# Kernel optimization log

Hardware: AMD Instinct MI355X
Metric: run time of the kernel (lower is better)

## Reference

```python
import jax, jax.numpy as jnp
import numpy as np

NT, NTR, NQ = 2048, 4096, 257  # time samples, traces, quantile knots


def cumtrapz(y, dx):
    # cumulative trapezoid along last axis, zero-prepended (preserve_dims=True)
    c = jnp.cumsum((y[..., 1:] + y[..., :-1]) * (0.5 * dx), axis=-1)
    return jnp.concatenate([jnp.zeros_like(y[..., :1]), c], axis=-1)


def trapz(y, dx):
    return (jnp.sum(y, axis=-1) - 0.5 * (y[..., 0] + y[..., -1])) * dx


def renorm(f, dx):
    # square + normalize to a pdf along time (standard W2-FWI renormalization)
    g = f * f
    return g / trapz(g, dx)[..., None]


def true_quantile(pdf, x, p, dx):
    # step-function quantile: invert clipped CDF via searchsorted per trace
    cdf = jnp.clip(cumtrapz(pdf, dx), 0.0, 1.0)  # [B, nt]
    idx = jax.vmap(lambda c: jnp.searchsorted(c, p))(cdf)  # [B, nq]
    idx = jnp.clip(idx, 0, x.shape[0] - 1)
    return x[idx]  # [B, nq]


def natural_cubic_coeffs(p, q):
    # batched natural cubic spline of q(p); knots p shared across batch
    h = p[1:] - p[:-1]                                 # [n-1]
    slope = (q[..., 1:] - q[..., :-1]) / h             # [B, n-1]
    rhs = 6.0 * (slope[..., 1:] - slope[..., :-1])     # [B, n-2]
    diag = 2.0 * (h[:-1] + h[1:])
    off = h[1:-1]
    T = jnp.diag(diag) + jnp.diag(off, 1) + jnp.diag(off, -1)  # [n-2, n-2], shared
    M_inner = jnp.linalg.solve(T, rhs[..., None])[..., 0]      # [B, n-2]
    z = jnp.zeros_like(q[..., :1])
    M = jnp.concatenate([z, M_inner, z], axis=-1)      # natural BCs: M0 = Mn = 0
    a = q[..., :-1]
    b = slope - h * (2.0 * M[..., :-1] + M[..., 1:]) / 6.0
    c = 0.5 * M[..., :-1]
    d = (M[..., 1:] - M[..., :-1]) / (6.0 * h)
    return a, b, c, d  # each [B, n-1]


def spline_eval(p, a, b, c, d, tq):
    # vectorized batched spline evaluation (replaces per-element Python loop)
    idx = jnp.clip(jnp.searchsorted(p, tq, side='left') - 1, 0, p.shape[0] - 2)
    frac = tq - p[idx]
    ga = jnp.take_along_axis(a, idx, axis=-1)
    gb = jnp.take_along_axis(b, idx, axis=-1)
    gc = jnp.take_along_axis(c, idx, axis=-1)
    gd = jnp.take_along_axis(d, idx, axis=-1)
    return ga + frac * (gb + frac * (gc + frac * gd))


def w2_forward(f, obs_data, t, p):
    dx = t[1] - t[0]
    # constructor-time part: quantile splines of observed data
    q = true_quantile(renorm(obs_data, dx), t, p, dx)   # [B, nq]
    a, b, c, d = natural_cubic_coeffs(p, q)
    # forward: CDF of synthetic, composed with observed quantile
    F = cumtrapz(renorm(f, dx), dx)                     # [B, nt]
    off_diag = spline_eval(p, a, b, c, d, F)            # [B, nt]
    diff = (t[None, :] - off_diag) ** 2
    integrated = trapz(diff * f, dx)                    # [B]
    return jnp.sum(integrated)


def setup_inputs() -> dict:
    key = jax.random.key(0)
    k1, k2 = jax.random.split(key)
    f = jax.random.normal(k1, (NTR, NT), dtype=jnp.float32)
    obs_data = jax.random.normal(k2, (NTR, NT), dtype=jnp.float32)
    t = jnp.linspace(0.0, 2.0, NT, dtype=jnp.float32)
    p = jnp.linspace(0.0, 1.0, NQ, dtype=jnp.float32)
    return {"f": f, "obs_data": obs_data, "t": t, "p": p}


def reference(f, obs_data, t, p):
    return w2_forward(f, obs_data, t, p)
```

## Files before the change

### kernel.cpp

```cpp
#include <hip/hip_runtime.h>

#define TPB 256
#define NT_ 2048
#define NQ_ 257
#define EPT 8
#define BW 16
#define BD (2*BW+1)
#define BAND_BYTES (BD*256*4)
#define H_P 0.00390625f
#define RTPB 1024

__device__ __forceinline__ double shfl_down_f64(double x, int off) {
  union { double d; int i[2]; } u; u.d = x;
  u.i[0] = __shfl_down(u.i[0], off, 64);
  u.i[1] = __shfl_down(u.i[1], off, 64);
  return u.d;
}

template<int CTRL, int RM, int BM, bool BC>
__device__ __forceinline__ float dppf(float x) {
  return __int_as_float(__builtin_amdgcn_update_dpp(
      0, __float_as_int(x), CTRL, RM, BM, BC));
}
template<int CTRL, int RM, int BM, bool BC>
__device__ __forceinline__ double dppd(double x) {
  union { double d; int i[2]; } u, o; u.d = x;
  o.i[0] = __builtin_amdgcn_update_dpp(0, u.i[0], CTRL, RM, BM, BC);
  o.i[1] = __builtin_amdgcn_update_dpp(0, u.i[1], CTRL, RM, BM, BC);
  return o.d;
}
__device__ __forceinline__ void iscan2(float& a, float& b) {
  a += dppf<0x111,0xF,0xF,true >(a);  b += dppf<0x111,0xF,0xF,true >(b);
  a += dppf<0x112,0xF,0xF,true >(a);  b += dppf<0x112,0xF,0xF,true >(b);
  a += dppf<0x114,0xF,0xF,true >(a);  b += dppf<0x114,0xF,0xF,true >(b);
  a += dppf<0x118,0xF,0xF,true >(a);  b += dppf<0x118,0xF,0xF,true >(b);
  a += dppf<0x142,0xa,0xF,false>(a);  b += dppf<0x142,0xa,0xF,false>(b);
  a += dppf<0x143,0xc,0xF,false>(a);  b += dppf<0x143,0xc,0xF,false>(b);
}
__device__ __forceinline__ void iscan2d(double& a, double& b) {
  a += dppd<0x111,0xF,0xF,true >(a);  b += dppd<0x111,0xF,0xF,true >(b);
  a += dppd<0x112,0xF,0xF,true >(a);  b += dppd<0x112,0xF,0xF,true >(b);
  a += dppd<0x114,0xF,0xF,true >(a);  b += dppd<0x114,0xF,0xF,true >(b);
  a += dppd<0x118,0xF,0xF,true >(a);  b += dppd<0x118,0xF,0xF,true >(b);
  a += dppd<0x142,0xa,0xF,false>(a);  b += dppd<0x142,0xa,0xF,false>(b);
  a += dppd<0x143,0xc,0xF,false>(a);  b += dppd<0x143,0xc,0xF,false>(b);
}

__global__ void w2_setup(float* __restrict__ bandS) {
  __shared__ double sh_L[256];
  __shared__ double sh_winv[256];
  const int tid = threadIdx.x;
  if (tid < 255) {
    double d, dm;
    if (tid >= 20) {
      d = dm = 3.7320508075688772935;
    } else {
      d = 4.0; dm = 0.0;
      for (int i = 1; i <= tid; i++) { dm = d; d = 4.0 - 1.0 / d; }
    }
    sh_winv[tid] = 256.0 / d;
    sh_L[tid] = (tid == 0) ? 0.0 : 1.0 / dm;
  }
  __syncthreads();
  const int j = tid;
  const double H = (double)H_P;
  if (j < 255) {
    double y[BW + 1];
    y[0] = 1.0;
    #pragma unroll
    for (int m = 1; m <= BW; m++) {
      int i = j + m;
      y[m] = (i <= 254) ? (-sh_L[i] * y[m - 1]) : 0.0;
    }
    double xn = 0.0;
    #pragma unroll
    for (int m = BW; m >= 0; m--) {
      int i = j + m;
      double val = 0.0;
      if (i <= 254) {
        double num = y[m] - ((i < 254) ? H * xn : 0.0);
        val = num * sh_winv[i];
        xn = val;
      }
      bandS[(m + BW) * 256 + j] = (float)val;
    }
    #pragma unroll
    for (int m = -1; m >= -BW; m--) {
      int i = j + m;
      double val = 0.0;
      if (i >= 0) {
        val = (-H * xn) * sh_winv[i];
        xn = val;
      }
      bandS[(m + BW) * 256 + j] = (float)val;
    }
  } else {
    for (int mm = 0; mm < BD; mm++) bandS[mm * 256 + j] = 0.0f;
  }
}

__global__ __launch_bounds__(TPB) void w2_main(
    const float* __restrict__ f, const float* __restrict__ obs,
    const float* __restrict__ t, const float* __restrict__ bandS,
    double* __restrict__ row_out) {
  __shared__ float s_qA[NQ_], s_qB[NQ_];
  __shared__ float s_rhsA[255 + 2 * BW], s_rhsB[255 + 2 * BW];
  __shared__ float s_MA[NQ_], s_MB[NQ_];
  __shared__ float4 s_coefA[256], s_coefB[256];
  __shared__ float s_wfA[4], s_wfB[4], s_wf2A[4], s_wf2B[4];
  __shared__ double s_wdA[4], s_wdB[4];
  __shared__ double s_miscA[2], s_miscB[2];

  const int tid = threadIdx.x;
  const int lane = tid & 63;
  const int wid = tid >> 6;
  const int rowA = (int)blockIdx.x * 2;
  const int rowB = rowA + 1;
  const int base = tid * EPT;
  const int emax = (tid == TPB - 1) ? EPT - 1 : EPT;

  const double dx = (double)t[1] - (double)t[0];

  float tl[EPT + 1];
  {
    const float4 a = *reinterpret_cast<const float4*>(t + base);
    const float4 b = *reinterpret_cast<const float4*>(t + base + 4);
    tl[0] = a.x; tl[1] = a.y; tl[2] = a.z; tl[3] = a.w;
    tl[4] = b.x; tl[5] = b.y; tl[6] = b.z; tl[7] = b.w;
  }
  tl[EPT] = (tid < TPB - 1) ? t[base + EPT] : 0.0f;

  float sAA[EPT], sAB[EPT];
  float epA = 0.0f, epB = 0.0f;
  {
    const float* orA = obs + (size_t)rowA * NT_;
    const float* orB = obs + (size_t)rowB * NT_;
    float ovA[EPT + 1], ovB[EPT + 1];
    {
      const float4 a0 = *reinterpret_cast<const float4*>(orA + base);
      const float4 a1 = *reinterpret_cast<const float4*>(orA + base + 4);
      const float4 b0 = *reinterpret_cast<const float4*>(orB + base);
      const float4 b1 = *reinterpret_cast<const float4*>(orB + base + 4);
      ovA[0] = a0.x; ovA[1] = a0.y; ovA[2] = a0.z; ovA[3] = a0.w;
      ovA[4] = a1.x; ovA[5] = a1.y; ovA[6] = a1.z; ovA[7] = a1.w;
      ovB[0] = b0.x; ovB[1] = b0.y; ovB[2] = b0.z; ovB[3] = b0.w;
      ovB[4] = b1.x; ovB[5] = b1.y; ovB[6] = b1.z; ovB[7] = b1.w;
    }
    ovA[EPT] = (tid < TPB - 1) ? orA[base + EPT] : 0.0f;
    ovB[EPT] = (tid < TPB - 1) ? orB[base + EPT] : 0.0f;
    for (int k = 0; k < emax; k++) {
      sAA[k] = ovA[k] * ovA[k] + ovA[k + 1] * ovA[k + 1];
      sAB[k] = ovB[k] * ovB[k] + ovB[k + 1] * ovB[k + 1];
      epA += sAA[k];
      epB += sAB[k];
    }
    if (emax < EPT) { sAA[EPT - 1] = 0.0f; sAB[EPT - 1] = 0.0f; }
  }
  float vA = epA, vB = epB;
  iscan2(vA, vB);
  float exclA = __shfl_up(vA, 1, 64);
  float exclB = __shfl_up(vB, 1, 64);
  if (lane == 0) { exclA = 0.0f; exclB = 0.0f; }
  if (lane == 63) { s_wfA[wid] = vA; s_wfB[wid] = vB; }
  __syncthreads();
  float woffA = 0.0f, totA = 0.0f, woffB = 0.0f, totB = 0.0f;
  #pragma unroll
  for (int w = 0; w < 4; w++) {
    float swA = s_wfA[w], swB = s_wfB[w];
    if (w < wid) { woffA += swA; woffB += swB; }
    totA += swA; totB += swB;
  }
  float runA = woffA + exclA, inclA = woffA + vA, invA = 1.0f / totA;
  float runB = woffB + exclB, inclB = woffB + vB, invB = 1.0f / totB;

  {
    float cprev = fminf(runA * invA, 1.0f);
    int j = (int)(cprev * 256.0f) + 1;
    float r = runA;
    for (int k = 0; k < emax; k++) {
      float cu_uns = (k == emax - 1) ? inclA : (r + sAA[k]);
      r = cu_uns;
      float cuc = fminf(cu_uns * invA, 1.0f);
      int jh = (int)(cuc * 256.0f);
      float tq = tl[k + 1];
      for (; j <= jh; j++) s_qA[j] = tq;
    }
    if (tid == 0) s_qA[0] = tl[0];
    if (tid == TPB - 1) {
      float tq = tl[EPT - 1];
      for (; j <= 256; j++) s_qA[j] = tq;
    }
  }
  {
    float cprev = fminf(runB * invB, 1.0f);
    int j = (int)(cprev * 256.0f) + 1;
    float r = runB;
    for (int k = 0; k < emax; k++) {
      float cu_uns = (k == emax - 1) ? inclB : (r + sAB[k]);
      r = cu_uns;
      float cuc = fminf(cu_uns * invB, 1.0f);
      int jh = (int)(cuc * 256.0f);
      float tq = tl[k + 1];
      for (; j <= jh; j++) s_qB[j] = tq;
    }
    if (tid == 0) s_qB[0] = tl[0];
    if (tid == TPB - 1) {
      float tq = tl[EPT - 1];
      for (; j <= 256; j++) s_qB[j] = tq;
    }
  }

  const float* frA = f + (size_t)rowA * NT_;
  const float* frB = f + (size_t)rowB * NT_;
  float fvA[EPT + 1], fvB[EPT + 1];
  {
    const float4 a0 = *reinterpret_cast<const float4*>(frA + base);
    const float4 a1 = *reinterpret_cast<const float4*>(frA + base + 4);
    const float4 b0 = *reinterpret_cast<const float4*>(frB + base);
    const float4 b1 = *reinterpret_cast<const float4*>(frB + base + 4);
    fvA[0] = a0.x; fvA[1] = a0.y; fvA[2] = a0.z; fvA[3] = a0.w;
    fvA[4] = a1.x; fvA[5] = a1.y; fvA[6] = a1.z; fvA[7] = a1.w;
    fvB[0] = b0.x; fvB[1] = b0.y; fvB[2] = b0.z; fvB[3] = b0.w;
    fvB[4] = b1.x; fvB[5] = b1.y; fvB[6] = b1.z; fvB[7] = b1.w;
  }
  fvA[EPT] = (tid < TPB - 1) ? frA[base + EPT] : 0.0f;
  fvB[EPT] = (tid < TPB - 1) ? frB[base + EPT] : 0.0f;

  float sBA[EPT], sBB[EPT];
  float ep2A = 0.0f, ep2B = 0.0f;
  for (int k = 0; k < emax; k++) {
    sBA[k] = fvA[k] * fvA[k] + fvA[k + 1] * fvA[k + 1];
    sBB[k] = fvB[k] * fvB[k] + fvB[k + 1] * fvB[k + 1];
    ep2A += sBA[k];
    ep2B += sBB[k];
  }
  if (emax < EPT) { sBA[EPT - 1] = 0.0f; sBB[EPT - 1] = 0.0f; }
  float v2A = ep2A, v2B = ep2B;
  iscan2(v2A, v2B);
  float excl2A = __shfl_up(v2A, 1, 64);
  float excl2B = __shfl_up(v2B, 1, 64);
  if (lane == 0) { excl2A = 0.0f; excl2B = 0.0f; }
  if (lane == 63) { s_wf2A[wid] = v2A; s_wf2B[wid] = v2B; }
  __syncthreads();

  float woff2A = 0.0f, tot2A = 0.0f, woff2B = 0.0f, tot2B = 0.0f;
  #pragma unroll
  for (int w = 0; w < 4; w++) {
    float swA = s_wf2A[w], swB = s_wf2B[w];
    if (w < wid) { woff2A += swA; woff2B += swB; }
    tot2A += swA; tot2B += swB;
  }
  float run2A = woff2A + excl2A, inv2A = 1.0f / tot2A;
  float run2B = woff2B + excl2B, inv2B = 1.0f / tot2B;

  if (tid < 255) {
    float sl0A = (s_qA[tid + 1] - s_qA[tid]) * 256.0f;
    float sl1A = (s_qA[tid + 2] - s_qA[tid + 1]) * 256.0f;
    s_rhsA[BW + tid] = 6.0f * (sl1A - sl0A);
    float sl0B = (s_qB[tid + 1] - s_qB[tid]) * 256.0f;
    float sl1B = (s_qB[tid + 2] - s_qB[tid + 1]) * 256.0f;
    s_rhsB[BW + tid] = 6.0f * (sl1B - sl0B);
  }
  if (tid < BW) { s_rhsA[tid] = 0.0f; s_rhsB[tid] = 0.0f; }
  if (tid >= TPB - BW) {
    s_rhsA[tid + (2 * BW - 1)] = 0.0f;
    s_rhsB[tid + (2 * BW - 1)] = 0.0f;
  }
  __syncthreads();

  float MregA = 0.0f, MregB = 0.0f;
  if (tid < 255) {
    #pragma unroll 11
    for (int dd = 0; dd < BD; dd++) {
      float w = bandS[dd * 256 + tid];
      MregA += w * s_rhsA[tid + dd];
      MregB += w * s_rhsB[tid + dd];
    }
  }
  if (tid < 255) { s_MA[tid + 1] = MregA; s_MB[tid + 1] = MregB; }
  if (tid == 0) { s_MA[0] = 0.0f; s_MA[256] = 0.0f; s_MB[0] = 0.0f; s_MB[256] = 0.0f; }
  __syncthreads();

  {
    const float h = H_P;
    float q0A = s_qA[tid], q1A = s_qA[tid + 1];
    float MiA = s_MA[tid], Mi1A = s_MA[tid + 1];
    float slA = (q1A - q0A) * 256.0f;
    float bA = slA - h * (2.0f * MiA + Mi1A) * (1.0f / 6.0f);
    s_coefA[tid] = make_float4(q0A, bA, 0.5f * MiA, (Mi1A - MiA) * (256.0f / 6.0f));
    float q0B = s_qB[tid], q1B = s_qB[tid + 1];
    float MiB = s_MB[tid], Mi1B = s_MB[tid + 1];
    float slB = (q1B - q0B) * 256.0f;
    float bB = slB - h * (2.0f * MiB + Mi1B) * (1.0f / 6.0f);
    s_coefB[tid] = make_float4(q0B, bB, 0.5f * MiB, (Mi1B - MiB) * (256.0f / 6.0f));
  }
  __syncthreads();

  double wsumA = 0.0, wsumB = 0.0;
  {
    float r2A = run2A, r2B = run2B;
    #pragma unroll
    for (int k = 0; k < EPT; k++) {
      if (k > 0) { r2A += sBA[k - 1]; r2B += sBB[k - 1]; }
      float FA = r2A * inv2A;
      float FB = r2B * inv2B;
      int idxA = (int)ceilf(FA * 256.0f) - 1;
      int idxB = (int)ceilf(FB * 256.0f) - 1;
      if (idxA < 0) idxA = 0; if (idxA > 255) idxA = 255;
      if (idxB < 0) idxB = 0; if (idxB > 255) idxB = 255;
      float fracA = FA - (float)idxA * H_P;
      float fracB = FB - (float)idxB * H_P;
      float4 cfA = s_coefA[idxA];
      float4 cfB = s_coefB[idxB];
      float valA = cfA.x + fracA * (cfA.y + fracA * (cfA.z + fracA * cfA.w));
      float valB = cfB.x + fracB * (cfB.y + fracB * (cfB.z + fracB * cfB.w));
      float diffA = tl[k] - valA;
      float diffB = tl[k] - valB;
      float wvA = diffA * diffA * fvA[k];
      float wvB = diffB * diffB * fvB[k];
      if (tid == 0 && k == 0) { s_miscA[0] = (double)wvA; s_miscB[0] = (double)wvB; }
      if (tid == TPB - 1 && k == EPT - 1) { s_miscA[1] = (double)wvA; s_miscB[1] = (double)wvB; }
      wsumA += (double)wvA;
      wsumB += (double)wvB;
    }
  }
  double rA = wsumA, rB = wsumB;
  iscan2d(rA, rB);
  if (lane == 63) { s_wdA[wid] = rA; s_wdB[wid] = rB; }
  __syncthreads();
  if (tid == 0) {
    double totwA = s_wdA[0] + s_wdA[1] + s_wdA[2] + s_wdA[3];
    double totwB = s_wdB[0] + s_wdB[1] + s_wdB[2] + s_wdB[3];
    row_out[rowA] = (totwA - 0.5 * (s_miscA[0] + s_miscA[1])) * dx;
    row_out[rowB] = (totwB - 0.5 * (s_miscB[0] + s_miscB[1])) * dx;
  }
}

__global__ __launch_bounds__(RTPB) void w2_reduce(const double* __restrict__ row_out,
                                                  int ntr, float* __restrict__ out) {
  __shared__ double s[RTPB / 64];
  int tid = threadIdx.x, lane = tid & 63, wid = tid >> 6;
  double v = 0.0;
  for (int i = tid; i < ntr; i += RTPB) v += row_out[i];
  #pragma unroll
  for (int off = 32; off >= 1; off >>= 1) v += shfl_down_f64(v, off);
  if (lane == 0) s[wid] = v;
  __syncthreads();
  if (tid == 0) {
    double tot = 0.0;
    #pragma unroll
    for (int i = 0; i < RTPB / 64; i++) tot += s[i];
    out[0] = (float)tot;
  }
}

extern "C" void kernel_launch(void* const* d_in, const int* in_sizes, int n_in,
                              void* d_out, int out_size, void* d_ws, size_t ws_size,
                              hipStream_t stream) {
  const float* f   = (const float*)d_in[0];
  const float* obs = (const float*)d_in[1];
  const float* t   = (const float*)d_in[2];
  int nt = in_sizes[2];
  int ntr = in_sizes[0] / nt;

  float* bandS = (float*)d_ws;
  double* rows = (double*)((char*)d_ws + BAND_BYTES);

  hipLaunchKernelGGL(w2_setup, dim3(1), dim3(256), 0, stream, bandS);
  hipLaunchKernelGGL(w2_main, dim3(ntr / 2), dim3(TPB), 0, stream,
                     f, obs, t, bandS, rows);
  hipLaunchKernelGGL(w2_reduce, dim3(1), dim3(RTPB), 0, stream,
                     rows, ntr, (float*)d_out);
}
```

Baseline: 42.38 us.

## Precompute banded inverse at compile time, halve bandwidth, accumulate weights in float

The banded approximate inverse of the spline tridiagonal matrix is now built at compile time with constexpr and stored in constant memory, so the separate setup kernel launch is gone. The band half-width drops from 16 to 8, which halves the per-thread multiply-adds in the spline second-derivative solve, and that loop is now fully unrolled. Per-thread weighted sums are accumulated in float instead of double, saving conversions and FP64 adds. The risks are extra truncation error from the narrower band (off-diagonal decay factor about 0.27 per step) and slightly lower accumulation precision.

Result: faster. 36.29 us (-14.4%).

```diff
diff --git a/kernel.cpp b/kernel.cpp
--- a/kernel.cpp
+++ b/kernel.cpp
@@ -4,11 +4,55 @@
 #define NT_ 2048
 #define NQ_ 257
 #define EPT 8
-#define BW 16
+#define BW 8
 #define BD (2*BW+1)
-#define BAND_BYTES (BD*256*4)
 #define H_P 0.00390625f
 #define RTPB 1024
+
+struct Band { float v[BD * 256]; };
+constexpr Band make_band() {
+  Band b{};
+  double L[256] = {}, winv[256] = {};
+  const double H = 1.0 / 256.0;
+  double w = 4.0 * H;
+  winv[0] = 1.0 / w;
+  L[0] = 0.0;
+  for (int i = 1; i < 255; i++) {
+    L[i] = H * winv[i - 1];
+    w = 4.0 * H - L[i] * H;
+    winv[i] = 1.0 / w;
+  }
+  for (int j = 0; j < 255; j++) {
+    double y[BW + 1] = {};
+    y[0] = 1.0;
+    for (int m = 1; m <= BW; m++) {
+      int i = j + m;
+      y[m] = (i <= 254) ? (-L[i] * y[m - 1]) : 0.0;
+    }
+    double xn = 0.0;
+    for (int m = BW; m >= 0; m--) {
+      int i = j + m;
+      double val = 0.0;
+      if (i <= 254) {
+        double num = y[m] - ((i < 254) ? H * xn : 0.0);
+        val = num * winv[i];
+        xn = val;
+      }
+      b.v[(m + BW) * 256 + j] = (float)val;
+    }
+    for (int m = -1; m >= -BW; m--) {
+      int i = j + m;
+      double val = 0.0;
+      if (i >= 0) {
+        val = (-H * xn) * winv[i];
+        xn = val;
+      }
+      b.v[(m + BW) * 256 + j] = (float)val;
+    }
+  }
+  return b;
+}
+__device__ __constant__ Band g_band = make_band();
 
 __device__ __forceinline__ double shfl_down_f64(double x, int off) {
   union { double d; int i[2]; } u; u.d = x;
@@ -46,63 +90,9 @@
   a += dppd<0x143,0xc,0xF,false>(a);  b += dppd<0x143,0xc,0xF,false>(b);
 }
 
-__global__ void w2_setup(float* __restrict__ bandS) {
-  __shared__ double sh_L[256];
-  __shared__ double sh_winv[256];
-  const int tid = threadIdx.x;
-  if (tid < 255) {
-    double d, dm;
-    if (tid >= 20) {
-      d = dm = 3.7320508075688772935;
-    } else {
-      d = 4.0; dm = 0.0;
-      for (int i = 1; i <= tid; i++) { dm = d; d = 4.0 - 1.0 / d; }
-    }
-    sh_winv[tid] = 256.0 / d;
-    sh_L[tid] = (tid == 0) ? 0.0 : 1.0 / dm;
-  }
-  __syncthreads();
-  const int j = tid;
-  const double H = (double)H_P;
-  if (j < 255) {
-    double y[BW + 1];
-    y[0] = 1.0;
-    #pragma unroll
-    for (int m = 1; m <= BW; m++) {
-      int i = j + m;
-      y[m] = (i <= 254) ? (-sh_L[i] * y[m - 1]) : 0.0;
-    }
-    double xn = 0.0;
-    #pragma unroll
-    for (int m = BW; m >= 0; m--) {
-      int i = j + m;
-      double val = 0.0;
-      if (i <= 254) {
-        double num = y[m] - ((i < 254) ? H * xn : 0.0);
-        val = num * sh_winv[i];
-        xn = val;
-      }
-      bandS[(m + BW) * 256 + j] = (float)val;
-    }
-    #pragma unroll
-    for (int m = -1; m >= -BW; m--) {
-      int i = j + m;
-      double val = 0.0;
-      if (i >= 0) {
-        val = (-H * xn) * sh_winv[i];
-        xn = val;
-      }
-      bandS[(m + BW) * 256 + j] = (float)val;
-    }
-  } else {
-    for (int mm = 0; mm < BD; mm++) bandS[mm * 256 + j] = 0.0f;
-  }
-}
-
 __global__ __launch_bounds__(TPB) void w2_main(
     const float* __restrict__ f, const float* __restrict__ obs,
-    const float* __restrict__ t, const float* __restrict__ bandS,
-    double* __restrict__ row_out) {
+    const float* __restrict__ t, double* __restrict__ row_out) {
   __shared__ float s_qA[NQ_], s_qB[NQ_];
   __shared__ float s_rhsA[255 + 2 * BW], s_rhsB[255 + 2 * BW];
   __shared__ float s_MA[NQ_], s_MB[NQ_];
@@ -270,9 +260,9 @@
 
   float MregA = 0.0f, MregB = 0.0f;
   if (tid < 255) {
-    #pragma unroll 11
+    #pragma unroll
     for (int dd = 0; dd < BD; dd++) {
-      float w = bandS[dd * 256 + tid];
+      float w = g_band.v[dd * 256 + tid];
       MregA += w * s_rhsA[tid + dd];
       MregB += w * s_rhsB[tid + dd];
     }
@@ -296,7 +286,7 @@
   }
   __syncthreads();
 
-  double wsumA = 0.0, wsumB = 0.0;
+  float csumA = 0.0f, csumB = 0.0f;
   {
     float r2A = run2A, r2B = run2B;
     #pragma unroll
@@ -320,11 +310,11 @@
       float wvB = diffB * diffB * fvB[k];
       if (tid == 0 && k == 0) { s_miscA[0] = (double)wvA; s_miscB[0] = (double)wvB; }
       if (tid == TPB - 1 && k == EPT - 1) { s_miscA[1] = (double)wvA; s_miscB[1] = (double)wvB; }
-      wsumA += (double)wvA;
-      wsumB += (double)wvB;
-    }
-  }
-  double rA = wsumA, rB = wsumB;
+      csumA += wvA;
+      csumB += wvB;
+    }
+  }
+  double rA = (double)csumA, rB = (double)csumB;
   iscan2d(rA, rB);
   if (lane == 63) { s_wdA[wid] = rA; s_wdB[wid] = rB; }
   __syncthreads();
@@ -363,12 +353,10 @@
   int nt = in_sizes[2];
   int ntr = in_sizes[0] / nt;
 
-  float* bandS = (float*)d_ws;
-  double* rows = (double*)((char*)d_ws + BAND_BYTES);
-
-  hipLaunchKernelGGL(w2_setup, dim3(1), dim3(256), 0, stream, bandS);
+  double* rows = (double*)d_ws;
+
   hipLaunchKernelGGL(w2_main, dim3(ntr / 2), dim3(TPB), 0, stream,
-                     f, obs, t, bandS, rows);
+                     f, obs, t, rows);
   hipLaunchKernelGGL(w2_reduce, dim3(1), dim3(RTPB), 0, stream,
                      rows, ntr, (float*)d_out);
 }
```
